# Kernel optimization log

Measured on AMD Instinct MI355X. Metric: run time of the kernel, lower is better.

Reference implementation:

```python
import jax, jax.numpy as jnp
import numpy as np

N_NODES = 100000
N_EDGES = 1200000
N_GRAPHS = 1000
NUM_SHAPES, NUM_COLORS, NUM_CLASSES = 16, 8, 10


def setup_inputs() -> dict:
    key = jax.random.key(0)
    ks = jax.random.split(key, 12)
    x = jax.random.randint(ks[0], (N_NODES, 2), 0, 8, dtype=jnp.int32)
    edge_index = jax.random.randint(ks[1], (2, N_EDGES), 0, N_NODES, dtype=jnp.int32)
    batch = jnp.sort(jax.random.randint(ks[2], (N_NODES,), 0, N_GRAPHS, dtype=jnp.int32))
    s = 0.05
    params = {
        "shape_emb": jax.random.normal(ks[3], (NUM_SHAPES, 8), jnp.float32) * s,
        "color_emb": jax.random.normal(ks[4], (NUM_COLORS, 8), jnp.float32) * s,
        "W_pre": jax.random.normal(ks[5], (32, 16), jnp.float32) * s,
        "b_pre": jnp.zeros((32,), jnp.float32),
        "W_rel1": jax.random.normal(ks[6], (64, 32), jnp.float32) * s,
        "b_rel1": jnp.zeros((64,), jnp.float32),
        "W_root1": jax.random.normal(ks[7], (64, 32), jnp.float32) * s,
        "W_rel2": jax.random.normal(ks[8], (64, 64), jnp.float32) * s,
        "b_rel2": jnp.zeros((64,), jnp.float32),
        "W_root2": jax.random.normal(ks[9], (64, 64), jnp.float32) * s,
        "W_cls": jax.random.normal(ks[10], (NUM_CLASSES, 64), jnp.float32) * s,
        "b_cls": jnp.zeros((NUM_CLASSES,), jnp.float32),
    }
    return dict(x=x, edge_index=edge_index, batch=batch, num_graphs=N_GRAPHS, **params)


def _graph_conv(h, src, dst, W_rel, b_rel, W_root, n_nodes):
    # PyG GraphConv: out = lin_rel(sum_{j in N(i)} x_j) + lin_root(x_i)
    agg = jax.ops.segment_sum(h[src], dst, num_segments=n_nodes)  # [N, d_in]
    return agg @ W_rel.T + b_rel + h @ W_root.T


def reference(x, edge_index, batch, num_graphs,
              shape_emb, color_emb, W_pre, b_pre,
              W_rel1, b_rel1, W_root1, W_rel2, b_rel2, W_root2,
              W_cls, b_cls):
    n_nodes = x.shape[0]
    src, dst = edge_index[0], edge_index[1]
    h = jnp.concatenate([shape_emb[x[:, 0]], color_emb[x[:, 1]]], axis=1)  # [N, 16]
    h = jax.nn.relu(h @ W_pre.T + b_pre)                                    # [N, 32]
    h = jax.nn.relu(_graph_conv(h, src, dst, W_rel1, b_rel1, W_root1, n_nodes))  # [N, 64]
    h = jax.nn.relu(_graph_conv(h, src, dst, W_rel2, b_rel2, W_root2, n_nodes))  # [N, 64]
    # global mean pool over graphs
    sums = jax.ops.segment_sum(h, batch, num_segments=num_graphs)           # [G, 64]
    counts = jax.ops.segment_sum(jnp.ones((n_nodes,), h.dtype), batch, num_segments=num_graphs)
    pooled = sums / jnp.maximum(counts, 1.0)[:, None]
    return pooled @ W_cls.T + b_cls                                         # [G, num_classes]
```

## Files before the change

kernel.cpp:

```cpp
#include <hip/hip_runtime.h>
#include <hip/hip_bf16.h>


#define NGRAPHS 1000
#define SCAN_CHUNK 4096
#define SRCMASK 0x1FFFF

typedef _Float16 f16x8 __attribute__((ext_vector_type(8)));
typedef float f32x4 __attribute__((ext_vector_type(4)));

__global__ __launch_bounds__(256) void k_hist(const int* __restrict__ dst,
                                              unsigned* __restrict__ hist16,
                                              int* __restrict__ rank, int nE)
{
    int e = blockIdx.x * 256 + threadIdx.x;
    if (e >= nE) return;
    int d = dst[e];
    int sh = (d & 1) * 16;
    unsigned old = atomicAdd(&hist16[d >> 1], 1u << sh);
    rank[e] = (old >> sh) & 0xffff;
}

__global__ __launch_bounds__(256) void k_scan_part(const unsigned* __restrict__ hist16,
                                                   int* __restrict__ bsum, int n)
{
    __shared__ int s[256];
    int t = threadIdx.x;
    int beg = blockIdx.x * SCAN_CHUNK + t * 16;
    int sum = 0;
#pragma unroll
    for (int q = 0; q < 16; q += 2) {
        int i = beg + q;
        if (i < n) {
            unsigned w = hist16[i >> 1];
            sum += (w & 0xffff);
            if (i + 1 < n) sum += (w >> 16);
        }
    }
    s[t] = sum;
    __syncthreads();
    for (int off = 128; off > 0; off >>= 1) {
        if (t < off) s[t] += s[t + off];
        __syncthreads();
    }
    if (t == 0) bsum[blockIdx.x] = s[0];
}

__global__ __launch_bounds__(64) void k_scan_mid(const int* __restrict__ bsum,
                                                 int* __restrict__ boffs,
                                                 int* __restrict__ row_ptr,
                                                 int B, int n)
{
    if (threadIdx.x == 0) {
        int run = 0;
        for (int b = 0; b < B; ++b) {
            boffs[b] = run;
            run += bsum[b];
        }
        row_ptr[n] = run;
    }
}

__global__ __launch_bounds__(256) void k_scan_apply(const unsigned* __restrict__ hist16,
                                                    const int* __restrict__ boffs,
                                                    int* __restrict__ row_ptr, int n)
{
    __shared__ int s[256];
    int t = threadIdx.x;
    int beg = blockIdx.x * SCAN_CHUNK + t * 16;
    int v[16];
    int sum = 0;
#pragma unroll
    for (int q = 0; q < 16; q += 2) {
        int i = beg + q;
        unsigned w = (i < n) ? hist16[i >> 1] : 0u;
        v[q] = (i < n) ? (int)(w & 0xffff) : 0;
        v[q + 1] = (i + 1 < n) ? (int)(w >> 16) : 0;
        sum += v[q] + v[q + 1];
    }
    s[t] = sum;
    __syncthreads();
    for (int off = 1; off < 256; off <<= 1) {
        int x = (t >= off) ? s[t - off] : 0;
        __syncthreads();
        s[t] += x;
        __syncthreads();
    }
    int base = boffs[blockIdx.x] + ((t == 0) ? 0 : s[t - 1]);
#pragma unroll
    for (int q = 0; q < 16; ++q) {
        int i = beg + q;
        if (i < n) {
            row_ptr[i] = base;
            base += v[q];
        }
    }
}

__global__ __launch_bounds__(256) void k_scatteridx(
    const int* __restrict__ src, const int* __restrict__ dst,
    const int* __restrict__ x, const int* __restrict__ row_ptr,
    const int* __restrict__ rank, int* __restrict__ sorted, int nE)
{
    int e = blockIdx.x * 256 + threadIdx.x;
    if (e >= nE) return;
    int d = dst[e];
    int s = src[e];
    int2 xv = *(const int2*)(x + 2 * s);
    int c = (xv.x << 3) | (xv.y & 7);
    sorted[row_ptr[d] + rank[e]] = (c << 17) | s;
}

__global__ __launch_bounds__(128) void k_table(
    const float* __restrict__ shape_emb, const float* __restrict__ color_emb,
    const float* __restrict__ W_pre, const float* __restrict__ b_pre,
    _Float16* __restrict__ table)
{
    int c = threadIdx.x;
    int si = c >> 3, ci = c & 7;
    float in[16];
#pragma unroll
    for (int k = 0; k < 8; ++k) in[k] = shape_emb[si * 8 + k];
#pragma unroll
    for (int k = 0; k < 8; ++k) in[8 + k] = color_emb[ci * 8 + k];
    float acc[32];
#pragma unroll
    for (int j = 0; j < 32; ++j) acc[j] = b_pre[j];
#pragma unroll
    for (int k = 0; k < 16; ++k) {
        float v = in[k];
#pragma unroll
        for (int j = 0; j < 32; ++j) acc[j] += W_pre[j * 16 + k] * v;
    }
#pragma unroll
    for (int g = 0; g < 4; ++g) {
        f16x8 o;
#pragma unroll
        for (int q = 0; q < 8; ++q) o[q] = (_Float16)fmaxf(acc[g * 8 + q], 0.f);
        *(f16x8*)(table + (size_t)c * 32 + g * 8) = o;
    }
}

__global__ __launch_bounds__(256) void k_fused1(
    const int* __restrict__ row_ptr, const int* __restrict__ sorted,
    const int* __restrict__ x, const _Float16* __restrict__ table,
    const float* __restrict__ W_rel, const float* __restrict__ b_rel,
    const float* __restrict__ W_root, _Float16* __restrict__ out, int n)
{
    __shared__ _Float16 tab[128 * 32];
    int t = threadIdx.x;
    for (int i = t * 8; i < 128 * 32; i += 2048)
        *(f16x8*)(tab + i) = *(const f16x8*)(table + i);

    int lane = t & 63;
    int w = t >> 6;
    int col = lane & 15;
    int krow = lane >> 4;

    f16x8 B[2][4];
#pragma unroll
    for (int ks = 0; ks < 2; ++ks) {
#pragma unroll
        for (int ct = 0; ct < 4; ++ct) {
            int j = ct * 16 + col;
            const float* srcw = (ks == 0 ? W_rel : W_root) + (size_t)j * 32 + krow * 8;
            float4 w0 = *(const float4*)(srcw);
            float4 w1 = *(const float4*)(srcw + 4);
            f16x8 bb;
            bb[0] = (_Float16)w0.x; bb[1] = (_Float16)w0.y;
            bb[2] = (_Float16)w0.z; bb[3] = (_Float16)w0.w;
            bb[4] = (_Float16)w1.x; bb[5] = (_Float16)w1.y;
            bb[6] = (_Float16)w1.z; bb[7] = (_Float16)w1.w;
            B[ks][ct] = bb;
        }
        __builtin_amdgcn_sched_barrier(0);
    }
    float bias[4];
#pragma unroll
    for (int ct = 0; ct < 4; ++ct) bias[ct] = b_rel[ct * 16 + col];

    __syncthreads();

    int nodebase = blockIdx.x * 128 + w * 32;
    f32x4 acc[2][4];
#pragma unroll
    for (int nt = 0; nt < 2; ++nt)
#pragma unroll
        for (int ct = 0; ct < 4; ++ct) acc[nt][ct] = (f32x4){0.f, 0.f, 0.f, 0.f};

#pragma unroll
    for (int nt = 0; nt < 2; ++nt) {
        int i = nodebase + nt * 16 + col;
        int iC = min(i, n - 1);
        int e0 = row_ptr[iC];
        int e1 = (i < n) ? row_ptr[iC + 1] : e0;

        float a[8] = {0, 0, 0, 0, 0, 0, 0, 0};
        int e = e0;
        for (; e + 2 <= e1; e += 2) {
            int c0 = sorted[e] >> 17;
            int c1 = sorted[e + 1] >> 17;
            f16x8 r0 = *(const f16x8*)(tab + c0 * 32 + krow * 8);
            f16x8 r1 = *(const f16x8*)(tab + c1 * 32 + krow * 8);
#pragma unroll
            for (int q = 0; q < 8; ++q) a[q] += (float)r0[q] + (float)r1[q];
        }
        if (e < e1) {
            int c0 = sorted[e] >> 17;
            f16x8 r0 = *(const f16x8*)(tab + c0 * 32 + krow * 8);
#pragma unroll
            for (int q = 0; q < 8; ++q) a[q] += (float)r0[q];
        }
        f16x8 Aagg;
#pragma unroll
        for (int q = 0; q < 8; ++q) Aagg[q] = (_Float16)a[q];

        int2 xv = *(const int2*)(x + 2 * (size_t)iC);
        int code = (xv.x << 3) | (xv.y & 7);
        f16x8 Aroot = *(const f16x8*)(tab + code * 32 + krow * 8);

#pragma unroll
        for (int ct = 0; ct < 4; ++ct)
            acc[nt][ct] = __builtin_amdgcn_mfma_f32_16x16x32_f16(
                Aagg, B[0][ct], acc[nt][ct], 0, 0, 0);
#pragma unroll
        for (int ct = 0; ct < 4; ++ct)
            acc[nt][ct] = __builtin_amdgcn_mfma_f32_16x16x32_f16(
                Aroot, B[1][ct], acc[nt][ct], 0, 0, 0);
    }

#pragma unroll
    for (int nt = 0; nt < 2; ++nt) {
#pragma unroll
        for (int r = 0; r < 4; ++r) {
            int node = nodebase + nt * 16 + krow * 4 + r;
            if (node < n) {
#pragma unroll
                for (int ct = 0; ct < 4; ++ct) {
                    float v = acc[nt][ct][r] + bias[ct];
                    out[(size_t)node * 64 + ct * 16 + col] = (_Float16)fmaxf(v, 0.f);
                }
            }
        }
    }
}

template <int WIDTH, int PARTS>
__global__ __launch_bounds__(256) void k_agg(
    const int* __restrict__ row_ptr, const int* __restrict__ sorted,
    const _Float16* __restrict__ h, _Float16* __restrict__ agg, int n)
{
    int tid = blockIdx.x * 256 + threadIdx.x;
    int i = tid / PARTS;
    int p = tid % PARTS;
    if (i >= n) return;
    float a[8] = {0, 0, 0, 0, 0, 0, 0, 0};
    float b[8] = {0, 0, 0, 0, 0, 0, 0, 0};
    int e0 = row_ptr[i], e1 = row_ptr[i + 1];
    const _Float16* hp = h + p * 8;
    int e = e0;
    for (; e + 4 <= e1; e += 4) {
        int s0 = sorted[e] & SRCMASK;
        int s1 = sorted[e + 1] & SRCMASK;
        int s2 = sorted[e + 2] & SRCMASK;
        int s3 = sorted[e + 3] & SRCMASK;
        f16x8 r0 = *(const f16x8*)(hp + (size_t)s0 * WIDTH);
        f16x8 r1 = *(const f16x8*)(hp + (size_t)s1 * WIDTH);
        f16x8 r2 = *(const f16x8*)(hp + (size_t)s2 * WIDTH);
        f16x8 r3 = *(const f16x8*)(hp + (size_t)s3 * WIDTH);
#pragma unroll
        for (int q = 0; q < 8; ++q) {
            a[q] += (float)r0[q] + (float)r2[q];
            b[q] += (float)r1[q] + (float)r3[q];
        }
    }
    for (; e < e1; ++e) {
        int s0 = sorted[e] & SRCMASK;
        f16x8 r0 = *(const f16x8*)(hp + (size_t)s0 * WIDTH);
#pragma unroll
        for (int q = 0; q < 8; ++q) a[q] += (float)r0[q];
    }
    f16x8 o;
#pragma unroll
    for (int q = 0; q < 8; ++q) o[q] = (_Float16)(a[q] + b[q]);
    *(f16x8*)(agg + (size_t)i * WIDTH + p * 8) = o;
}

template <int WIN>
__global__ __launch_bounds__(256) void k_conv_mfma(
    const _Float16* __restrict__ agg, const _Float16* __restrict__ h,
    const float* __restrict__ W_rel, const float* __restrict__ b_rel,
    const float* __restrict__ W_root, _Float16* __restrict__ out, int n)
{
    constexpr int NK = (2 * WIN) / 32;
    int t = threadIdx.x;
    int lane = t & 63;
    int w = t >> 6;
    int col = lane & 15;
    int krow = lane >> 4;

    f16x8 B[NK][4];
#pragma unroll
    for (int ks = 0; ks < NK; ++ks) {
#pragma unroll
        for (int ct = 0; ct < 4; ++ct) {
            int j = ct * 16 + col;
            int kb = ks * 32 + krow * 8;
            const float* srcw = (ks < NK / 2)
                ? (W_rel + (size_t)j * WIN + kb)
                : (W_root + (size_t)j * WIN + (kb - WIN));
            float4 w0 = *(const float4*)(srcw);
            float4 w1 = *(const float4*)(srcw + 4);
            f16x8 bb;
            bb[0] = (_Float16)w0.x; bb[1] = (_Float16)w0.y;
            bb[2] = (_Float16)w0.z; bb[3] = (_Float16)w0.w;
            bb[4] = (_Float16)w1.x; bb[5] = (_Float16)w1.y;
            bb[6] = (_Float16)w1.z; bb[7] = (_Float16)w1.w;
            B[ks][ct] = bb;
        }
        __builtin_amdgcn_sched_barrier(0);
    }

    float bias[4];
#pragma unroll
    for (int ct = 0; ct < 4; ++ct) bias[ct] = b_rel[ct * 16 + col];

    int nodebase = blockIdx.x * 128 + w * 32;

    f32x4 acc[2][4];
#pragma unroll
    for (int nt = 0; nt < 2; ++nt)
#pragma unroll
        for (int ct = 0; ct < 4; ++ct) acc[nt][ct] = (f32x4){0.f, 0.f, 0.f, 0.f};

#pragma unroll
    for (int ks = 0; ks < NK; ++ks) {
        const _Float16* base = (ks < NK / 2) ? agg : h;
        int koff = ((ks < NK / 2) ? ks : ks - NK / 2) * 32 + krow * 8;
#pragma unroll
        for (int nt = 0; nt < 2; ++nt) {
            int i = nodebase + nt * 16 + col;
            i = min(i, n - 1);
            f16x8 a = *(const f16x8*)(base + (size_t)i * WIN + koff);
#pragma unroll
            for (int ct = 0; ct < 4; ++ct)
                acc[nt][ct] = __builtin_amdgcn_mfma_f32_16x16x32_f16(
                    a, B[ks][ct], acc[nt][ct], 0, 0, 0);
        }
    }

#pragma unroll
    for (int nt = 0; nt < 2; ++nt) {
#pragma unroll
        for (int r = 0; r < 4; ++r) {
            int node = nodebase + nt * 16 + krow * 4 + r;
            if (node < n) {
#pragma unroll
                for (int ct = 0; ct < 4; ++ct) {
                    float v = acc[nt][ct][r] + bias[ct];
                    out[(size_t)node * 64 + ct * 16 + col] = (_Float16)fmaxf(v, 0.f);
                }
            }
        }
    }
}

__global__ __launch_bounds__(256) void k_pool_cls(
    const _Float16* __restrict__ h3, const int* __restrict__ batch,
    const float* __restrict__ W_cls, const float* __restrict__ b_cls,
    float* __restrict__ out, int n)
{
    __shared__ float part[4][64];
    __shared__ float pool[64];
    __shared__ int range[2];
    int g = blockIdx.x;
    int t = threadIdx.x;

    if (t < 2) {
        int key = g + t;
        int lo = 0, hi = n;
        while (lo < hi) {
            int mid = (lo + hi) >> 1;
            if (batch[mid] < key) lo = mid + 1; else hi = mid;
        }
        range[t] = lo;
    }
    __syncthreads();
    int start = range[0], end = range[1];

    int j = t & 63;
    int sub = t >> 6;
    float local = 0.f;
    for (int i = start + sub; i < end; i += 4)
        local += (float)h3[(size_t)i * 64 + j];
    part[sub][j] = local;
    __syncthreads();

    if (t < 64) {
        float cnt = (float)(end - start);
        float inv = 1.0f / fmaxf(cnt, 1.0f);
        pool[t] = (part[0][t] + part[1][t] + part[2][t] + part[3][t]) * inv;
    }
    __syncthreads();

    if (t < 10) {
        float acc = b_cls[t];
#pragma unroll
        for (int k = 0; k < 64; ++k) acc += W_cls[t * 64 + k] * pool[k];
        out[(size_t)g * 10 + t] = acc;
    }
}

extern "C" void kernel_launch(void* const* d_in, const int* in_sizes, int n_in,
                              void* d_out, int out_size, void* d_ws, size_t ws_size,
                              hipStream_t stream)
{
    const int* x        = (const int*)d_in[0];
    const int* ei       = (const int*)d_in[1];
    const int* batch    = (const int*)d_in[2];
    const float* shape_emb = (const float*)d_in[4];
    const float* color_emb = (const float*)d_in[5];
    const float* W_pre   = (const float*)d_in[6];
    const float* b_pre   = (const float*)d_in[7];
    const float* W_rel1  = (const float*)d_in[8];
    const float* b_rel1  = (const float*)d_in[9];
    const float* W_root1 = (const float*)d_in[10];
    const float* W_rel2  = (const float*)d_in[11];
    const float* b_rel2  = (const float*)d_in[12];
    const float* W_root2 = (const float*)d_in[13];
    const float* W_cls   = (const float*)d_in[14];
    const float* b_cls   = (const float*)d_in[15];

    const int n  = in_sizes[0] / 2;
    const int nE = in_sizes[1] / 2;
    const int G  = NGRAPHS;
    const int* src = ei;
    const int* dst = ei + nE;

    _Float16* us = (_Float16*)d_ws;
    _Float16* h2B   = us;
    _Float16* agg2B = us + (size_t)n * 64;
    _Float16* h3B   = us + (size_t)n * 128;
    _Float16* tabB  = us + (size_t)n * 192;
    int* ints    = (int*)(tabB + 128 * 32);
    int* row_ptr = ints;
    unsigned* hist16 = (unsigned*)(row_ptr + (n + 1));
    int* rank    = (int*)(hist16 + (n / 2 + 1));
    int* sorted  = rank + nE;
    int* bsum    = sorted + nE;
    int* boffs   = bsum + 64;

    const int EB = (nE + 255) / 256;
    const int CB = (n + 127) / 128;
    const int SB = (n + SCAN_CHUNK - 1) / SCAN_CHUNK;

    hipMemsetAsync(hist16, 0, (size_t)(n / 2 + 1) * sizeof(unsigned), stream);
    k_table<<<1, 128, 0, stream>>>(shape_emb, color_emb, W_pre, b_pre, tabB);
    k_hist<<<EB, 256, 0, stream>>>(dst, hist16, rank, nE);
    k_scan_part<<<SB, 256, 0, stream>>>(hist16, bsum, n);
    k_scan_mid<<<1, 64, 0, stream>>>(bsum, boffs, row_ptr, SB, n);
    k_scan_apply<<<SB, 256, 0, stream>>>(hist16, boffs, row_ptr, n);
    k_scatteridx<<<EB, 256, 0, stream>>>(src, dst, x, row_ptr, rank, sorted, nE);

    k_fused1<<<CB, 256, 0, stream>>>(row_ptr, sorted, x, tabB,
                                     W_rel1, b_rel1, W_root1, h2B, n);
    k_agg<64, 8><<<((size_t)n * 8 + 255) / 256, 256, 0, stream>>>(row_ptr, sorted, h2B, agg2B, n);
    k_conv_mfma<64><<<CB, 256, 0, stream>>>(agg2B, h2B, W_rel2, b_rel2, W_root2, h3B, n);
    k_pool_cls<<<G, 256, 0, stream>>>(h3B, batch, W_cls, b_cls, (float*)d_out, n);
}
```

Baseline: 279.7 us.

## Replace global-atomic CSR build with two-pass LDS bucket radix partition

```diff
diff --git a/kernel.cpp b/kernel.cpp
--- a/kernel.cpp
+++ b/kernel.cpp
@@ -4,37 +4,45 @@
 
 #define NGRAPHS 1000
 #define SCAN_CHUNK 4096
+#define EPB 4096
 #define SRCMASK 0x1FFFF
 
 typedef _Float16 f16x8 __attribute__((ext_vector_type(8)));
 typedef float f32x4 __attribute__((ext_vector_type(4)));
 
-__global__ __launch_bounds__(256) void k_hist(const int* __restrict__ dst,
-                                              unsigned* __restrict__ hist16,
-                                              int* __restrict__ rank, int nE)
-{
-    int e = blockIdx.x * 256 + threadIdx.x;
-    if (e >= nE) return;
-    int d = dst[e];
-    int sh = (d & 1) * 16;
-    unsigned old = atomicAdd(&hist16[d >> 1], 1u << sh);
-    rank[e] = (old >> sh) & 0xffff;
-}
-
-__global__ __launch_bounds__(256) void k_scan_part(const unsigned* __restrict__ hist16,
-                                                   int* __restrict__ bsum, int n)
+__global__ __launch_bounds__(256) void k_bcount(const int* __restrict__ dst,
+                                                int* __restrict__ cnt,
+                                                int nE, int nbuck)
+{
+    __shared__ int h[512];
+    int t = threadIdx.x;
+    for (int i = t; i < nbuck; i += 256) h[i] = 0;
+    __syncthreads();
+    int base = blockIdx.x * EPB;
+#pragma unroll
+    for (int q = 0; q < 16; ++q) {
+        int e = base + q * 256 + t;
+        if (e < nE) atomicAdd(&h[dst[e] >> 8], 1);
+    }
+    __syncthreads();
+    int* out = cnt + (size_t)blockIdx.x * nbuck;
+    for (int i = t; i < nbuck; i += 256) out[i] = h[i];
+}
+
+__global__ __launch_bounds__(256) void k_pscan_part(const int* __restrict__ cnt,
+                                                    int* __restrict__ bsum,
+                                                    int L, int nbuck, int nblka)
 {
     __shared__ int s[256];
     int t = threadIdx.x;
     int beg = blockIdx.x * SCAN_CHUNK + t * 16;
     int sum = 0;
 #pragma unroll
-    for (int q = 0; q < 16; q += 2) {
+    for (int q = 0; q < 16; ++q) {
         int i = beg + q;
-        if (i < n) {
-            unsigned w = hist16[i >> 1];
-            sum += (w & 0xffff);
-            if (i + 1 < n) sum += (w >> 16);
+        if (i < L) {
+            int b = i / nblka, k = i - b * nblka;
+            sum += cnt[(size_t)k * nbuck + b];
         }
     }
     s[t] = sum;
@@ -61,9 +69,10 @@
     }
 }
 
-__global__ __launch_bounds__(256) void k_scan_apply(const unsigned* __restrict__ hist16,
-                                                    const int* __restrict__ boffs,
-                                                    int* __restrict__ row_ptr, int n)
+__global__ __launch_bounds__(256) void k_pscan_apply(const int* __restrict__ cnt,
+                                                     const int* __restrict__ boffs,
+                                                     int* __restrict__ offs_flat,
+                                                     int L, int nbuck, int nblka)
 {
     __shared__ int s[256];
     int t = threadIdx.x;
@@ -71,44 +80,93 @@
     int v[16];
     int sum = 0;
 #pragma unroll
-    for (int q = 0; q < 16; q += 2) {
-        int i = beg + q;
-        unsigned w = (i < n) ? hist16[i >> 1] : 0u;
-        v[q] = (i < n) ? (int)(w & 0xffff) : 0;
-        v[q + 1] = (i + 1 < n) ? (int)(w >> 16) : 0;
-        sum += v[q] + v[q + 1];
-    }
-    s[t] = sum;
-    __syncthreads();
-    for (int off = 1; off < 256; off <<= 1) {
-        int x = (t >= off) ? s[t - off] : 0;
-        __syncthreads();
-        s[t] += x;
-        __syncthreads();
-    }
-    int base = boffs[blockIdx.x] + ((t == 0) ? 0 : s[t - 1]);
-#pragma unroll
     for (int q = 0; q < 16; ++q) {
         int i = beg + q;
-        if (i < n) {
-            row_ptr[i] = base;
+        if (i < L) {
+            int b = i / nblka, k = i - b * nblka;
+            v[q] = cnt[(size_t)k * nbuck + b];
+        } else v[q] = 0;
+        sum += v[q];
+    }
+    s[t] = sum;
+    __syncthreads();
+    for (int off = 1; off < 256; off <<= 1) {
+        int x2 = (t >= off) ? s[t - off] : 0;
+        __syncthreads();
+        s[t] += x2;
+        __syncthreads();
+    }
+    int base = boffs[blockIdx.x] + ((t == 0) ? 0 : s[t - 1]);
+#pragma unroll
+    for (int q = 0; q < 16; ++q) {
+        int i = beg + q;
+        if (i < L) {
+            offs_flat[i] = base;
             base += v[q];
         }
     }
 }
 
-__global__ __launch_bounds__(256) void k_scatteridx(
+__global__ __launch_bounds__(256) void k_bpart(
     const int* __restrict__ src, const int* __restrict__ dst,
-    const int* __restrict__ x, const int* __restrict__ row_ptr,
-    const int* __restrict__ rank, int* __restrict__ sorted, int nE)
-{
-    int e = blockIdx.x * 256 + threadIdx.x;
-    if (e >= nE) return;
-    int d = dst[e];
-    int s = src[e];
-    int2 xv = *(const int2*)(x + 2 * s);
-    int c = (xv.x << 3) | (xv.y & 7);
-    sorted[row_ptr[d] + rank[e]] = (c << 17) | s;
+    const int* __restrict__ x, const int* __restrict__ offs_flat,
+    unsigned* __restrict__ part, int nE, int nblka)
+{
+    __shared__ int h[512];
+    int t = threadIdx.x;
+    for (int i = t; i < 512; i += 256) h[i] = 0;
+    __syncthreads();
+    int base = blockIdx.x * EPB;
+#pragma unroll
+    for (int q = 0; q < 16; ++q) {
+        int e = base + q * 256 + t;
+        if (e < nE) {
+            int d = dst[e];
+            int b = d >> 8;
+            int r = atomicAdd(&h[b], 1);
+            int s = src[e];
+            int2 xv = *(const int2*)(x + 2 * (size_t)s);
+            unsigned code = (unsigned)((xv.x << 3) | (xv.y & 7));
+            unsigned payload = ((unsigned)(d & 255) << 24) | (code << 17) | (unsigned)s;
+            part[offs_flat[(size_t)b * nblka + blockIdx.x] + r] = payload;
+        }
+    }
+}
+
+__global__ __launch_bounds__(256) void k_bfinal(
+    const unsigned* __restrict__ part, const int* __restrict__ offs_flat,
+    int* __restrict__ row_ptr, int* __restrict__ sorted,
+    int n, int nbuck, int nblka, int nE)
+{
+    __shared__ int h[256];
+    __shared__ int cur[256];
+    int b = blockIdx.x;
+    int t = threadIdx.x;
+    int ebeg = offs_flat[(size_t)b * nblka];
+    int eend = (b + 1 < nbuck) ? offs_flat[(size_t)(b + 1) * nblka] : nE;
+
+    h[t] = 0;
+    __syncthreads();
+    for (int e = ebeg + t; e < eend; e += 256)
+        atomicAdd(&h[part[e] >> 24], 1);
+    __syncthreads();
+    int myv = h[t];
+    for (int off = 1; off < 256; off <<= 1) {
+        int x2 = (t >= off) ? h[t - off] : 0;
+        __syncthreads();
+        h[t] += x2;
+        __syncthreads();
+    }
+    int excl = h[t] - myv;
+    int node = b * 256 + t;
+    if (node < n) row_ptr[node] = ebeg + excl;
+    cur[t] = ebeg + excl;
+    __syncthreads();
+    for (int e = ebeg + t; e < eend; e += 256) {
+        unsigned u = part[e];
+        int r = atomicAdd(&cur[u >> 24], 1);
+        sorted[r] = (int)(u & 0xFFFFFFu);
+    }
 }
 
 __global__ __launch_bounds__(128) void k_table(
@@ -437,30 +495,35 @@
     const int* src = ei;
     const int* dst = ei + nE;
 
+    const int NBUCK = (n + 255) >> 8;
+    const int NBLKA = (nE + EPB - 1) / EPB;
+    const int L     = NBUCK * NBLKA;
+    const int SBL   = (L + SCAN_CHUNK - 1) / SCAN_CHUNK;
+
     _Float16* us = (_Float16*)d_ws;
     _Float16* h2B   = us;
     _Float16* agg2B = us + (size_t)n * 64;
     _Float16* h3B   = us + (size_t)n * 128;
     _Float16* tabB  = us + (size_t)n * 192;
-    int* ints    = (int*)(tabB + 128 * 32);
-    int* row_ptr = ints;
-    unsigned* hist16 = (unsigned*)(row_ptr + (n + 1));
-    int* rank    = (int*)(hist16 + (n / 2 + 1));
-    int* sorted  = rank + nE;
-    int* bsum    = sorted + nE;
-    int* boffs   = bsum + 64;
-
-    const int EB = (nE + 255) / 256;
+    int* ints      = (int*)(tabB + 128 * 32);
+    int* row_ptr   = ints;
+    int* cnt       = row_ptr + (n + 1);
+    int* offs_flat = cnt + L;
+    unsigned* part = (unsigned*)(offs_flat + L);
+    int* sorted    = (int*)(part + nE);
+    int* bsum      = sorted + nE;
+    int* boffs     = bsum + 64;
+
     const int CB = (n + 127) / 128;
-    const int SB = (n + SCAN_CHUNK - 1) / SCAN_CHUNK;
-
-    hipMemsetAsync(hist16, 0, (size_t)(n / 2 + 1) * sizeof(unsigned), stream);
+
     k_table<<<1, 128, 0, stream>>>(shape_emb, color_emb, W_pre, b_pre, tabB);
-    k_hist<<<EB, 256, 0, stream>>>(dst, hist16, rank, nE);
-    k_scan_part<<<SB, 256, 0, stream>>>(hist16, bsum, n);
-    k_scan_mid<<<1, 64, 0, stream>>>(bsum, boffs, row_ptr, SB, n);
-    k_scan_apply<<<SB, 256, 0, stream>>>(hist16, boffs, row_ptr, n);
-    k_scatteridx<<<EB, 256, 0, stream>>>(src, dst, x, row_ptr, rank, sorted, nE);
+    k_bcount<<<NBLKA, 256, 0, stream>>>(dst, cnt, nE, NBUCK);
+    k_pscan_part<<<SBL, 256, 0, stream>>>(cnt, bsum, L, NBUCK, NBLKA);
+    k_scan_mid<<<1, 64, 0, stream>>>(bsum, boffs, row_ptr, SBL, n);
+    k_pscan_apply<<<SBL, 256, 0, stream>>>(cnt, boffs, offs_flat, L, NBUCK, NBLKA);
+    k_bpart<<<NBLKA, 256, 0, stream>>>(src, dst, x, offs_flat, part, nE, NBLKA);
+    k_bfinal<<<NBUCK, 256, 0, stream>>>(part, offs_flat, row_ptr, sorted,
+                                        n, NBUCK, NBLKA, nE);
 
     k_fused1<<<CB, 256, 0, stream>>>(row_ptr, sorted, x, tabB,
                                      W_rel1, b_rel1, W_root1, h2B, n);
```

After: 253.8 us. 1.1x faster.
